# Kernel tuning notes

Measured on AMD Instinct MI355X. Metric: run time of the kernel, lower is better.

Reference implementation:

```python
import jax, jax.numpy as jnp
import numpy as np

B, D, P, E = 256, 512, 128, 128  # batch, in_dim, nproto, projection_dim

def setup_inputs() -> dict:
    key = jax.random.key(0)
    k1, k2 = jax.random.split(key)
    x = jax.random.normal(k1, (B, D, P), dtype=jnp.float32)
    # glorot-uniform-like weights, one [D,E] matrix per prototype
    limit = jnp.sqrt(6.0 / (D + E)).astype(jnp.float32)
    W = jax.random.uniform(k2, (P, D, E), dtype=jnp.float32, minval=-limit, maxval=limit)
    b = jnp.zeros((P, E), dtype=jnp.float32)  # bias per prototype
    return {"x": x, "W": W, "b": b}

def reference(x, W, b):
    # Original: for each proto p, x[:,:,p] @ W_p + b_p, stacked on axis=2.
    # Fused as a single batched GEMM over the prototype axis.
    # x: [B,D,P], W: [P,D,E] -> out: [B,E,P]
    out = jnp.einsum('bdp,pde->bep', x, W)
    out = out + b.T[None, :, :]  # b: [P,E] -> broadcast [1,E,P]
    return out
```

## Files before the change

kernel.cpp:

```cpp
#include <hip/hip_runtime.h>
#include <cstdint>
#include <cstddef>

#define B_ 256
#define D_ 512
#define P_ 128
#define E_ 128

typedef unsigned short u16;
typedef unsigned int   u32;
typedef __bf16  bf16x8_t __attribute__((ext_vector_type(8)));
typedef float   f32x4_t  __attribute__((ext_vector_type(4)));
typedef u16     u16x4_t  __attribute__((ext_vector_type(4)));
typedef u16     u16x8_t  __attribute__((ext_vector_type(8)));

__device__ __forceinline__ u16 f2bf(float f) {
  union { float f; unsigned int u; } c; c.f = f;
  unsigned int u = c.u;
  unsigned int r = (u + 0x7FFFu + ((u >> 16) & 1u)) >> 16;
  return (u16)r;
}
__device__ __forceinline__ float bf2f(u16 v) {
  union { unsigned int u; float f; } c; c.u = (unsigned int)v << 16;
  return c.f;
}

__global__ __launch_bounds__(256) void transpose_cvt2_kernel(
    const float* __restrict__ x, const float* __restrict__ W,
    u16* __restrict__ xT, u16* __restrict__ Wt) {
  __shared__ float tile[32][516];

  const int bid  = blockIdx.x;
  const bool isX = (bid < 1024);
  const int o    = isX ? (bid >> 2) : ((bid - 1024) >> 2);
  const int c0   = (bid & 3) * 32;
  const float* src = isX ? x : W;
  u16* dst = isX ? xT : Wt;
  const size_t rs = isX ? (size_t)(B_ * D_) : (size_t)D_;
  const size_t os = isX ? (size_t)D_ : (size_t)(E_ * D_);

  const int t = threadIdx.x;

  {
    const float* s = src + (size_t)o * (D_ * 128) + c0 + (t & 7) * 4;
    const int cl = (t & 7) * 4;
    #pragma unroll
    for (int j = 0; j < 16; ++j) {
      const int d = (t >> 3) + 32 * j;
      const float4 v = *reinterpret_cast<const float4*>(s + (size_t)d * 128);
      tile[cl + 0][d] = v.x; tile[cl + 1][d] = v.y;
      tile[cl + 2][d] = v.z; tile[cl + 3][d] = v.w;
    }
  }
  __syncthreads();

  {
    const int c = t >> 3;
    const int m = t & 7;
    u16* drow = dst + (size_t)(c0 + c) * rs + (size_t)o * os;
    #pragma unroll
    for (int it = 0; it < 8; ++it) {
      const int db = m * 8 + it * 64;
      u16x8_t pk;
      #pragma unroll
      for (int k = 0; k < 8; ++k) pk[k] = f2bf(tile[c][db + k]);
      *reinterpret_cast<u16x8_t*>(drow + db) = pk;
    }
  }
}


#define SWZ_ELEM(row, g) (((row) << 6) + ((((g) ^ ((row) & 7))) << 3))

__global__ __launch_bounds__(512, 2) void gemm_kernel(
    const u16* __restrict__ xT, const u16* __restrict__ Wt,
    const float* __restrict__ bias, u16* __restrict__ ws2) {
  __shared__ __attribute__((aligned(16))) u16 As[3][128 * 64];
  __shared__ __attribute__((aligned(16))) u16 Bs[3][128 * 64];

  const int wg  = blockIdx.x;
  const int xcd = wg & 7;
  const int i   = wg >> 3;
  const int p   = xcd * 16 + (i & 15);
  const int b0  = (i >> 4) * 128;

  const int t    = threadIdx.x;
  const int lane = t & 63;
  const int wv   = t >> 6;
  const int wr   = wv >> 2;
  const int wc   = wv & 3;

  const u16* Ag = xT + (size_t)p * (B_ * D_) + (size_t)b0 * D_;
  const u16* Bg = Wt + (size_t)p * (E_ * D_);

  const int r1 = t >> 3;
  const int sw = (((t & 7) ^ (r1 & 7)) << 3);

  const int fr = lane & 15;
  const int fq = lane >> 4;

  f32x4_t acc[4][2] = {};

#define GLOAD(gp, lp) __builtin_amdgcn_global_load_lds( \
    (const __attribute__((address_space(1))) void*)(gp), \
    (__attribute__((address_space(3))) void*)(lp), 16, 0, 0)

#define STAGE_AB(buf, d0) do { \
    GLOAD(Ag + (size_t)r1 * D_ + (d0) + sw,        &As[buf][wv * 512]); \
    GLOAD(Ag + (size_t)(r1 + 64) * D_ + (d0) + sw, &As[buf][4096 + wv * 512]); \
    GLOAD(Bg + (size_t)r1 * D_ + (d0) + sw,        &Bs[buf][wv * 512]); \
    GLOAD(Bg + (size_t)(r1 + 64) * D_ + (d0) + sw, &Bs[buf][4096 + wv * 512]); \
  } while (0)

#define MFMA(a, b, c) __builtin_amdgcn_mfma_f32_16x16x32_bf16((a), (b), (c), 0, 0, 0)

#define K_ITER(KT, BUF, PREFETCH, VMSTR, LAST) do { \
    bf16x8_t af[4][2], bfr[2][2]; \
    _Pragma("unroll") \
    for (int ii = 0; ii < 4; ++ii) { \
      const int rowa = wr * 64 + ii * 16 + fr; \
      af[ii][0] = *reinterpret_cast<const bf16x8_t*>(&As[BUF][SWZ_ELEM(rowa, fq)]); \
      af[ii][1] = *reinterpret_cast<const bf16x8_t*>(&As[BUF][SWZ_ELEM(rowa, 4 + fq)]); \
    } \
    _Pragma("unroll") \
    for (int jj = 0; jj < 2; ++jj) { \
      const int rowb = wc * 32 + jj * 16 + fr; \
      bfr[jj][0] = *reinterpret_cast<const bf16x8_t*>(&Bs[BUF][SWZ_ELEM(rowb, fq)]); \
      bfr[jj][1] = *reinterpret_cast<const bf16x8_t*>(&Bs[BUF][SWZ_ELEM(rowb, 4 + fq)]); \
    } \
    asm volatile("s_waitcnt lgkmcnt(0)" ::: "memory"); \
    __builtin_amdgcn_sched_barrier(0); \
    __builtin_amdgcn_s_barrier(); \
    if (PREFETCH) STAGE_AB(BUF, ((KT) + 3) * 64); \
    _Pragma("unroll") \
    for (int kh = 0; kh < 2; ++kh) \
      _Pragma("unroll") \
      for (int ii = 0; ii < 4; ++ii) \
        _Pragma("unroll") \
        for (int jj = 0; jj < 2; ++jj) \
          acc[ii][jj] = MFMA(af[ii][kh], bfr[jj][kh], acc[ii][jj]); \
    if (!(LAST)) { \
      asm volatile("s_waitcnt " VMSTR ::: "memory"); \
      __builtin_amdgcn_sched_barrier(0); \
      __builtin_amdgcn_s_barrier(); \
    } \
  } while (0)

  STAGE_AB(0, 0);
  STAGE_AB(1, 64);
  STAGE_AB(2, 128);
  asm volatile("s_waitcnt vmcnt(8)" ::: "memory");
  __builtin_amdgcn_sched_barrier(0);
  __builtin_amdgcn_s_barrier();

  K_ITER(0, 0, 1, "vmcnt(8)", 0);
  K_ITER(1, 1, 1, "vmcnt(8)", 0);
  K_ITER(2, 2, 1, "vmcnt(8)", 0);
  K_ITER(3, 0, 1, "vmcnt(8)", 0);
  K_ITER(4, 1, 1, "vmcnt(8)", 0);
  K_ITER(5, 2, 0, "vmcnt(4)", 0);
  K_ITER(6, 0, 0, "vmcnt(0)", 0);
  K_ITER(7, 1, 0, "vmcnt(0)", 1);

#undef K_ITER
#undef MFMA
#undef STAGE_AB
#undef GLOAD

  const int q4 = fq * 4;
  #pragma unroll
  for (int jj = 0; jj < 2; ++jj) {
    const int e  = wc * 32 + jj * 16 + fr;
    const float bv = bias[p * E_ + e];
    #pragma unroll
    for (int ii = 0; ii < 4; ++ii) {
      const int r0 = b0 + wr * 64 + ii * 16 + q4;
      #pragma unroll
      for (int rg = 0; rg < 4; ++rg) {
        ws2[((size_t)p * B_ + (r0 + rg)) * E_ + e] = f2bf(acc[ii][jj][rg] + bv);
      }
    }
  }
}

__global__ __launch_bounds__(256) void out_transpose_kernel(
    const u16* __restrict__ ws2, float* __restrict__ out) {
  __shared__ float tile[64][65];

  const int b  = blockIdx.x;
  const int p0 = blockIdx.y * 64;
  const int e0 = blockIdx.z * 64;
  const int t  = threadIdx.x;

  const u16* s = ws2 + ((size_t)p0 * B_ + b) * E_ + e0;

  {
    const int lr = t >> 4;
    const int lc = (t & 15) * 4;
    #pragma unroll
    for (int it = 0; it < 4; ++it) {
      const int r = lr + it * 16;
      const u16x4_t v = *reinterpret_cast<const u16x4_t*>(s + (size_t)r * (B_ * E_) + lc);
      tile[r][lc + 0] = bf2f(v[0]); tile[r][lc + 1] = bf2f(v[1]);
      tile[r][lc + 2] = bf2f(v[2]); tile[r][lc + 3] = bf2f(v[3]);
    }
  }
  __syncthreads();

  {
    const int c  = t >> 4;
    const int wd = (t & 15) * 4;
    #pragma unroll
    for (int it = 0; it < 4; ++it) {
      const int cc = c + it * 16;
      float4 v;
      v.x = tile[wd + 0][cc]; v.y = tile[wd + 1][cc];
      v.z = tile[wd + 2][cc]; v.w = tile[wd + 3][cc];
      *reinterpret_cast<float4*>(out + ((size_t)b * E_ + e0 + cc) * P_ + p0 + wd) = v;
    }
  }
}

__global__ __launch_bounds__(256) void naive_kernel(
    const float* __restrict__ x, const float* __restrict__ W,
    const float* __restrict__ bias, float* __restrict__ out) {
  const size_t idx = (size_t)blockIdx.x * 256 + threadIdx.x;
  const int p = (int)(idx & 127);
  const int e = (int)((idx >> 7) & 127);
  const int b = (int)(idx >> 14);
  float acc = bias[p * E_ + e];
  const float* xp = x + (size_t)b * D_ * P_ + p;
  const float* wp = W + (size_t)p * D_ * E_ + e;
  for (int d = 0; d < D_; ++d) acc += xp[(size_t)d * P_] * wp[(size_t)d * E_];
  out[idx] = acc;
}

extern "C" void kernel_launch(void* const* d_in, const int* in_sizes, int n_in,
                              void* d_out, int out_size, void* d_ws, size_t ws_size,
                              hipStream_t stream) {
  (void)in_sizes; (void)n_in; (void)out_size;
  const float* x    = (const float*)d_in[0];
  const float* W    = (const float*)d_in[1];
  const float* bias = (const float*)d_in[2];
  float* out = (float*)d_out;

  const size_t xT_bytes  = (size_t)P_ * B_ * D_ * 2;
  const size_t Wt_bytes  = (size_t)P_ * E_ * D_ * 2;
  const size_t ws2_bytes = (size_t)P_ * B_ * E_ * 2;

  if (ws_size < xT_bytes + Wt_bytes + ws2_bytes) {
    naive_kernel<<<dim3((B_ * E_ * P_) / 256), 256, 0, stream>>>(x, W, bias, out);
    return;
  }

  u16* xT  = (u16*)d_ws;
  u16* Wt  = (u16*)((char*)d_ws + xT_bytes);
  u16* ws2 = (u16*)((char*)d_ws + xT_bytes + Wt_bytes);

  transpose_cvt2_kernel<<<dim3(1536), 256, 0, stream>>>(x, W, xT, Wt);
  gemm_kernel<<<dim3(256), 512, 0, stream>>>(xT, Wt, bias, ws2);
  out_transpose_kernel<<<dim3(B_, 2, 2), 256, 0, stream>>>(ws2, out);
}
```

Baseline: 44.90 us.

## Replace shared-memory transpose with blocked 8-element bf16 layout for GEMM operands

The prep kernel no longer transposes x and W through LDS. It converts them to bf16 in a blocked layout [outer][d/8][128][8], where each 16-byte chunk holds 8 consecutive d values for one column. The GEMM's global-to-LDS loads are re-indexed to fetch these 16-byte chunks directly from the new layout, keeping the same LDS swizzle. This removes the LDS round-trip and barrier from the prep stage. In exchange, GEMM loads become 16-byte pieces strided across p, and prep loads are 4-byte scalar reads, which may reduce memory coalescing efficiency.

```diff
diff --git a/kernel.cpp b/kernel.cpp
--- a/kernel.cpp
+++ b/kernel.cpp
@@ -25,47 +25,33 @@
   return c.f;
 }
 
-__global__ __launch_bounds__(256) void transpose_cvt2_kernel(
+__global__ __launch_bounds__(256) void prep_kernel(
     const float* __restrict__ x, const float* __restrict__ W,
-    u16* __restrict__ xT, u16* __restrict__ Wt) {
-  __shared__ float tile[32][516];
-
+    u16* __restrict__ xB, u16* __restrict__ wB) {
   const int bid  = blockIdx.x;
   const bool isX = (bid < 1024);
-  const int o    = isX ? (bid >> 2) : ((bid - 1024) >> 2);
-  const int c0   = (bid & 3) * 32;
-  const float* src = isX ? x : W;
-  u16* dst = isX ? xT : Wt;
-  const size_t rs = isX ? (size_t)(B_ * D_) : (size_t)D_;
-  const size_t os = isX ? (size_t)D_ : (size_t)(E_ * D_);
-
-  const int t = threadIdx.x;
-
-  {
-    const float* s = src + (size_t)o * (D_ * 128) + c0 + (t & 7) * 4;
-    const int cl = (t & 7) * 4;
-    #pragma unroll
-    for (int j = 0; j < 16; ++j) {
-      const int d = (t >> 3) + 32 * j;
-      const float4 v = *reinterpret_cast<const float4*>(s + (size_t)d * 128);
-      tile[cl + 0][d] = v.x; tile[cl + 1][d] = v.y;
-      tile[cl + 2][d] = v.z; tile[cl + 3][d] = v.w;
-    }
-  }
-  __syncthreads();
-
-  {
-    const int c = t >> 3;
-    const int m = t & 7;
-    u16* drow = dst + (size_t)(c0 + c) * rs + (size_t)o * os;
-    #pragma unroll
-    for (int it = 0; it < 8; ++it) {
-      const int db = m * 8 + it * 64;
-      u16x8_t pk;
-      #pragma unroll
-      for (int k = 0; k < 8; ++k) pk[k] = f2bf(tile[c][db + k]);
-      *reinterpret_cast<u16x8_t*>(drow + db) = pk;
-    }
+  const int idx  = isX ? bid : (bid - 1024);
+  const int o    = idx >> 2;
+  const int dc0  = (idx & 3) * 16;
+
+  const float* src = (isX ? x : W) + (size_t)o * (D_ * 128);
+  u16* dst = (isX ? xB : wB) + (size_t)o * (64 * 128 * 8);
+
+  const int t   = threadIdx.x;
+  const int c   = t & 127;
+  const int dcL = t >> 7;
+
+  #pragma unroll
+  for (int it = 0; it < 8; ++it) {
+    const int dc = dc0 + dcL + 2 * it;
+    float v[8];
+    #pragma unroll
+    for (int j = 0; j < 8; ++j)
+      v[j] = src[(size_t)(dc * 8 + j) * 128 + c];
+    u16x8_t pk;
+    #pragma unroll
+    for (int j = 0; j < 8; ++j) pk[j] = f2bf(v[j]);
+    *reinterpret_cast<u16x8_t*>(dst + ((size_t)dc * 128 + c) * 8) = pk;
   }
 }
 
@@ -73,7 +59,7 @@
 #define SWZ_ELEM(row, g) (((row) << 6) + ((((g) ^ ((row) & 7))) << 3))
 
 __global__ __launch_bounds__(512, 2) void gemm_kernel(
-    const u16* __restrict__ xT, const u16* __restrict__ Wt,
+    const u16* __restrict__ xB, const u16* __restrict__ wB,
     const float* __restrict__ bias, u16* __restrict__ ws2) {
   __shared__ __attribute__((aligned(16))) u16 As[3][128 * 64];
   __shared__ __attribute__((aligned(16))) u16 Bs[3][128 * 64];
@@ -90,11 +76,8 @@
   const int wr   = wv >> 2;
   const int wc   = wv & 3;
 
-  const u16* Ag = xT + (size_t)p * (B_ * D_) + (size_t)b0 * D_;
-  const u16* Bg = Wt + (size_t)p * (E_ * D_);
-
   const int r1 = t >> 3;
-  const int sw = (((t & 7) ^ (r1 & 7)) << 3);
+  const int gs = (t & 7) ^ (r1 & 7);
 
   const int fr = lane & 15;
   const int fq = lane >> 4;
@@ -105,11 +88,11 @@
     (const __attribute__((address_space(1))) void*)(gp), \
     (__attribute__((address_space(3))) void*)(lp), 16, 0, 0)
 
-#define STAGE_AB(buf, d0) do { \
-    GLOAD(Ag + (size_t)r1 * D_ + (d0) + sw,        &As[buf][wv * 512]); \
-    GLOAD(Ag + (size_t)(r1 + 64) * D_ + (d0) + sw, &As[buf][4096 + wv * 512]); \
-    GLOAD(Bg + (size_t)r1 * D_ + (d0) + sw,        &Bs[buf][wv * 512]); \
-    GLOAD(Bg + (size_t)(r1 + 64) * D_ + (d0) + sw, &Bs[buf][4096 + wv * 512]); \
+#define STAGE_AB(buf, dc0) do { \
+    GLOAD(xB + (((size_t)(b0 + r1) * 64 + (dc0) + gs) * 128 + p) * 8,        &As[buf][wv * 512]); \
+    GLOAD(xB + (((size_t)(b0 + r1 + 64) * 64 + (dc0) + gs) * 128 + p) * 8,   &As[buf][4096 + wv * 512]); \
+    GLOAD(wB + (((size_t)p * 64 + (dc0) + gs) * 128 + r1) * 8,               &Bs[buf][wv * 512]); \
+    GLOAD(wB + (((size_t)p * 64 + (dc0) + gs) * 128 + r1 + 64) * 8,          &Bs[buf][4096 + wv * 512]); \
   } while (0)
 
 #define MFMA(a, b, c) __builtin_amdgcn_mfma_f32_16x16x32_bf16((a), (b), (c), 0, 0, 0)
@@ -131,7 +114,7 @@
     asm volatile("s_waitcnt lgkmcnt(0)" ::: "memory"); \
     __builtin_amdgcn_sched_barrier(0); \
     __builtin_amdgcn_s_barrier(); \
-    if (PREFETCH) STAGE_AB(BUF, ((KT) + 3) * 64); \
+    if (PREFETCH) STAGE_AB(BUF, ((KT) + 3) * 8); \
     _Pragma("unroll") \
     for (int kh = 0; kh < 2; ++kh) \
       _Pragma("unroll") \
@@ -147,8 +130,8 @@
   } while (0)
 
   STAGE_AB(0, 0);
-  STAGE_AB(1, 64);
-  STAGE_AB(2, 128);
+  STAGE_AB(1, 8);
+  STAGE_AB(2, 16);
   asm volatile("s_waitcnt vmcnt(8)" ::: "memory");
   __builtin_amdgcn_sched_barrier(0);
   __builtin_amdgcn_s_barrier();
@@ -244,20 +227,20 @@
   const float* bias = (const float*)d_in[2];
   float* out = (float*)d_out;
 
-  const size_t xT_bytes  = (size_t)P_ * B_ * D_ * 2;
-  const size_t Wt_bytes  = (size_t)P_ * E_ * D_ * 2;
+  const size_t xB_bytes  = (size_t)B_ * 64 * 128 * 8 * 2;
+  const size_t wB_bytes  = (size_t)P_ * 64 * 128 * 8 * 2;
   const size_t ws2_bytes = (size_t)P_ * B_ * E_ * 2;
 
-  if (ws_size < xT_bytes + Wt_bytes + ws2_bytes) {
+  if (ws_size < xB_bytes + wB_bytes + ws2_bytes) {
     naive_kernel<<<dim3((B_ * E_ * P_) / 256), 256, 0, stream>>>(x, W, bias, out);
     return;
   }
 
-  u16* xT  = (u16*)d_ws;
-  u16* Wt  = (u16*)((char*)d_ws + xT_bytes);
-  u16* ws2 = (u16*)((char*)d_ws + xT_bytes + Wt_bytes);
-
-  transpose_cvt2_kernel<<<dim3(1536), 256, 0, stream>>>(x, W, xT, Wt);
-  gemm_kernel<<<dim3(256), 512, 0, stream>>>(xT, Wt, bias, ws2);
+  u16* xB  = (u16*)d_ws;
+  u16* wB  = (u16*)((char*)d_ws + xB_bytes);
+  u16* ws2 = (u16*)((char*)d_ws + xB_bytes + wB_bytes);
+
+  prep_kernel<<<dim3(1536), 256, 0, stream>>>(x, W, xB, wB);
+  gemm_kernel<<<dim3(256), 512, 0, stream>>>(xB, wB, bias, ws2);
   out_transpose_kernel<<<dim3(B_, 2, 2), 256, 0, stream>>>(ws2, out);
 }
```

Result: slower. 51.11 us (+13.8%).

## Rewrite prep transpose with register bf16 packing; double-buffer GEMM LDS

Applied to the files above, without the earlier changes.

The fp32-to-bf16 transpose kernel is rewritten so each thread loads rows, packs bf16 pairs in registers and writes 16-byte chunks into a smaller, XOR-swizzled LDS tile. It then stores them as coalesced 16-byte chunks with occupancy hint 4. This cuts LDS footprint and scalar LDS traffic in the memory-bound prep stage. The d ordering inside each 8-element chunk is permuted, but identically for x and W, so the GEMM reduction is unchanged. The GEMM drops from triple to double buffering, which lowers LDS use but gives shallower prefetch depth and less latency hiding.

```diff
diff --git a/kernel.cpp b/kernel.cpp
--- a/kernel.cpp
+++ b/kernel.cpp
@@ -13,6 +13,7 @@
 typedef float   f32x4_t  __attribute__((ext_vector_type(4)));
 typedef u16     u16x4_t  __attribute__((ext_vector_type(4)));
 typedef u16     u16x8_t  __attribute__((ext_vector_type(8)));
+typedef u32     u32x4_t  __attribute__((ext_vector_type(4)));
 
 __device__ __forceinline__ u16 f2bf(float f) {
   union { float f; unsigned int u; } c; c.f = f;
@@ -20,51 +21,67 @@
   unsigned int r = (u + 0x7FFFu + ((u >> 16) & 1u)) >> 16;
   return (u16)r;
 }
+__device__ __forceinline__ u32 pk2bf(float a, float b) {
+  return (u32)f2bf(a) | ((u32)f2bf(b) << 16);
+}
 __device__ __forceinline__ float bf2f(u16 v) {
   union { unsigned int u; float f; } c; c.u = (unsigned int)v << 16;
   return c.f;
 }
 
-__global__ __launch_bounds__(256) void transpose_cvt2_kernel(
+__global__ __launch_bounds__(256, 4) void prep_kernel(
     const float* __restrict__ x, const float* __restrict__ W,
     u16* __restrict__ xT, u16* __restrict__ Wt) {
-  __shared__ float tile[32][516];
+  __shared__ __attribute__((aligned(16))) u32 lds[128 * 16 * 4];
 
   const int bid  = blockIdx.x;
   const bool isX = (bid < 1024);
-  const int o    = isX ? (bid >> 2) : ((bid - 1024) >> 2);
-  const int c0   = (bid & 3) * 32;
-  const float* src = isX ? x : W;
+  const int idx  = isX ? bid : (bid - 1024);
+  const int o    = idx >> 2;
+  const int dblk = idx & 3;
+  const float* src = (isX ? x : W) + (size_t)o * (D_ * 128) + (size_t)dblk * (128 * 128);
   u16* dst = isX ? xT : Wt;
-  const size_t rs = isX ? (size_t)(B_ * D_) : (size_t)D_;
-  const size_t os = isX ? (size_t)D_ : (size_t)(E_ * D_);
-
-  const int t = threadIdx.x;
+  const size_t crs = isX ? (size_t)(256 * 64) : (size_t)64;
+  const size_t ors = isX ? (size_t)64 : (size_t)(128 * 64);
+  const int kcG0 = dblk * 16;
+
+  const int t    = threadIdx.x;
+  const int wv   = t >> 6;
+  const int lane = t & 63;
+  const int c5   = lane & 31;
+  const int par  = lane >> 5;
+
+  #pragma unroll
+  for (int i2 = 0; i2 < 2; ++i2) {
+    const int dc16 = wv + 4 * i2;
+    f32x4_t v[8];
+    #pragma unroll
+    for (int j = 0; j < 8; ++j)
+      v[j] = *reinterpret_cast<const f32x4_t*>(
+          src + (size_t)(dc16 * 16 + 2 * j + par) * 128 + c5 * 4);
+    const int kcL = dc16 * 2 + par;
+    #pragma unroll
+    for (int q = 0; q < 4; ++q) {
+      const int p = 4 * c5 + q;
+      u32x4_t ch;
+      ch[0] = pk2bf(v[0][q], v[1][q]);
+      ch[1] = pk2bf(v[2][q], v[3][q]);
+      ch[2] = pk2bf(v[4][q], v[5][q]);
+      ch[3] = pk2bf(v[6][q], v[7][q]);
+      const int unit = p * 16 + (kcL ^ (c5 & 15));
+      *reinterpret_cast<u32x4_t*>(&lds[unit * 4]) = ch;
+    }
+  }
+  __syncthreads();
 
   {
-    const float* s = src + (size_t)o * (D_ * 128) + c0 + (t & 7) * 4;
-    const int cl = (t & 7) * 4;
-    #pragma unroll
-    for (int j = 0; j < 16; ++j) {
-      const int d = (t >> 3) + 32 * j;
-      const float4 v = *reinterpret_cast<const float4*>(s + (size_t)d * 128);
-      tile[cl + 0][d] = v.x; tile[cl + 1][d] = v.y;
-      tile[cl + 2][d] = v.z; tile[cl + 3][d] = v.w;
-    }
-  }
-  __syncthreads();
-
-  {
-    const int c = t >> 3;
-    const int m = t & 7;
-    u16* drow = dst + (size_t)(c0 + c) * rs + (size_t)o * os;
-    #pragma unroll
-    for (int it = 0; it < 8; ++it) {
-      const int db = m * 8 + it * 64;
-      u16x8_t pk;
-      #pragma unroll
-      for (int k = 0; k < 8; ++k) pk[k] = f2bf(tile[c][db + k]);
-      *reinterpret_cast<u16x8_t*>(drow + db) = pk;
+    const int kcL = t & 15;
+    #pragma unroll
+    for (int j = 0; j < 8; ++j) {
+      const int p = (t >> 4) + 16 * j;
+      const int unit = p * 16 + (kcL ^ ((p >> 2) & 15));
+      const u32x4_t ch = *reinterpret_cast<const u32x4_t*>(&lds[unit * 4]);
+      *reinterpret_cast<u32x4_t*>(dst + ((size_t)p * crs + (size_t)o * ors + kcG0 + kcL) * 8) = ch;
     }
   }
 }
@@ -75,8 +92,8 @@
 __global__ __launch_bounds__(512, 2) void gemm_kernel(
     const u16* __restrict__ xT, const u16* __restrict__ Wt,
     const float* __restrict__ bias, u16* __restrict__ ws2) {
-  __shared__ __attribute__((aligned(16))) u16 As[3][128 * 64];
-  __shared__ __attribute__((aligned(16))) u16 Bs[3][128 * 64];
+  __shared__ __attribute__((aligned(16))) u16 As[2][128 * 64];
+  __shared__ __attribute__((aligned(16))) u16 Bs[2][128 * 64];
 
   const int wg  = blockIdx.x;
   const int xcd = wg & 7;
@@ -114,24 +131,24 @@
 
 #define MFMA(a, b, c) __builtin_amdgcn_mfma_f32_16x16x32_bf16((a), (b), (c), 0, 0, 0)
 
-#define K_ITER(KT, BUF, PREFETCH, VMSTR, LAST) do { \
+#define K_ITER(KT, PREFETCH, VMSTR, LAST) do { \
     bf16x8_t af[4][2], bfr[2][2]; \
     _Pragma("unroll") \
     for (int ii = 0; ii < 4; ++ii) { \
       const int rowa = wr * 64 + ii * 16 + fr; \
-      af[ii][0] = *reinterpret_cast<const bf16x8_t*>(&As[BUF][SWZ_ELEM(rowa, fq)]); \
-      af[ii][1] = *reinterpret_cast<const bf16x8_t*>(&As[BUF][SWZ_ELEM(rowa, 4 + fq)]); \
+      af[ii][0] = *reinterpret_cast<const bf16x8_t*>(&As[(KT) & 1][SWZ_ELEM(rowa, fq)]); \
+      af[ii][1] = *reinterpret_cast<const bf16x8_t*>(&As[(KT) & 1][SWZ_ELEM(rowa, 4 + fq)]); \
     } \
     _Pragma("unroll") \
     for (int jj = 0; jj < 2; ++jj) { \
       const int rowb = wc * 32 + jj * 16 + fr; \
-      bfr[jj][0] = *reinterpret_cast<const bf16x8_t*>(&Bs[BUF][SWZ_ELEM(rowb, fq)]); \
-      bfr[jj][1] = *reinterpret_cast<const bf16x8_t*>(&Bs[BUF][SWZ_ELEM(rowb, 4 + fq)]); \
+      bfr[jj][0] = *reinterpret_cast<const bf16x8_t*>(&Bs[(KT) & 1][SWZ_ELEM(rowb, fq)]); \
+      bfr[jj][1] = *reinterpret_cast<const bf16x8_t*>(&Bs[(KT) & 1][SWZ_ELEM(rowb, 4 + fq)]); \
     } \
     asm volatile("s_waitcnt lgkmcnt(0)" ::: "memory"); \
     __builtin_amdgcn_sched_barrier(0); \
     __builtin_amdgcn_s_barrier(); \
-    if (PREFETCH) STAGE_AB(BUF, ((KT) + 3) * 64); \
+    if (PREFETCH) STAGE_AB((KT) & 1, ((KT) + 2) * 64); \
     _Pragma("unroll") \
     for (int kh = 0; kh < 2; ++kh) \
       _Pragma("unroll") \
@@ -148,19 +165,18 @@
 
   STAGE_AB(0, 0);
   STAGE_AB(1, 64);
-  STAGE_AB(2, 128);
-  asm volatile("s_waitcnt vmcnt(8)" ::: "memory");
+  asm volatile("s_waitcnt vmcnt(4)" ::: "memory");
   __builtin_amdgcn_sched_barrier(0);
   __builtin_amdgcn_s_barrier();
 
-  K_ITER(0, 0, 1, "vmcnt(8)", 0);
-  K_ITER(1, 1, 1, "vmcnt(8)", 0);
-  K_ITER(2, 2, 1, "vmcnt(8)", 0);
-  K_ITER(3, 0, 1, "vmcnt(8)", 0);
-  K_ITER(4, 1, 1, "vmcnt(8)", 0);
-  K_ITER(5, 2, 0, "vmcnt(4)", 0);
-  K_ITER(6, 0, 0, "vmcnt(0)", 0);
-  K_ITER(7, 1, 0, "vmcnt(0)", 1);
+  K_ITER(0, 1, "vmcnt(4)", 0);
+  K_ITER(1, 1, "vmcnt(4)", 0);
+  K_ITER(2, 1, "vmcnt(4)", 0);
+  K_ITER(3, 1, "vmcnt(4)", 0);
+  K_ITER(4, 1, "vmcnt(4)", 0);
+  K_ITER(5, 1, "vmcnt(4)", 0);
+  K_ITER(6, 0, "vmcnt(0)", 0);
+  K_ITER(7, 0, "vmcnt(0)", 1);
 
 #undef K_ITER
 #undef MFMA
@@ -257,7 +273,7 @@
   u16* Wt  = (u16*)((char*)d_ws + xT_bytes);
   u16* ws2 = (u16*)((char*)d_ws + xT_bytes + Wt_bytes);
 
-  transpose_cvt2_kernel<<<dim3(1536), 256, 0, stream>>>(x, W, xT, Wt);
+  prep_kernel<<<dim3(1536), 256, 0, stream>>>(x, W, xT, Wt);
   gemm_kernel<<<dim3(256), 512, 0, stream>>>(xT, Wt, bias, ws2);
   out_transpose_kernel<<<dim3(B_, 2, 2), 256, 0, stream>>>(ws2, out);
 }
```

Result: faster. 43.65 us (-2.8%).
